# Performance work log

Measured on AMD Instinct MI355X. Metric: run time of the kernel, lower is better.

## Reference

```python
import jax, jax.numpy as jnp
import numpy as np

B, N, DH, DG, HID, K_STEPS, CURV = 256, 2048, 128, 256, 256, 2, 1.0
SC = CURV ** 0.5
SCALE = 1.0 / (DH ** 0.5)
LN_EPS = 1e-5


def _artanh(x):
    return jnp.arctanh(jnp.clip(x, -1.0 + 1e-5, 1.0 - 1e-5))


def logmap0(x, sc=SC):
    n = jnp.maximum(jnp.linalg.norm(x, axis=-1, keepdims=True), 1e-7)
    return x * (_artanh(sc * n) / (sc * n))


def expmap0(v, sc=SC):
    n = jnp.maximum(jnp.linalg.norm(v, axis=-1, keepdims=True), 1e-7)
    return v * (jnp.tanh(sc * n) / (sc * n))


def setup_inputs() -> dict:
    key = jax.random.key(0)
    ks = jax.random.split(key, 16)

    def lin(k, out_d, in_d):
        return (jax.random.normal(k, (out_d, in_d), jnp.float32) * (in_d ** -0.5))

    demo_hyp = expmap0(0.1 * jax.random.normal(ks[0], (B, N, DH), jnp.float32))
    rho_g = jax.random.normal(ks[1], (B, DG), jnp.float32)
    return {
        "demo_hyp": demo_hyp,
        "rho_g": rho_g,
        "seed_g_w": lin(ks[2], DH, DG),
        "seed_g_b": jnp.zeros((DH,), jnp.float32),
        "seed_d_w": lin(ks[3], DH, DH),
        "pool_wq_w": lin(ks[4], DH, DH),
        "pool_wk_w": lin(ks[5], DH, DH),
        "pool_wv_w": lin(ks[6], DH, DH),
        "q_u_w": lin(ks[7], DH, DH),
        "q_g_w": lin(ks[8], DH, DG),
        "q_g_b": jnp.zeros((DH,), jnp.float32),
        "kv_w": lin(ks[9], DH, DH),
        "mlp_w1": lin(ks[10], HID, DH),
        "mlp_b1": jnp.zeros((HID,), jnp.float32),
        "mlp_w2": lin(ks[11], DH, HID),
        "mlp_b2": jnp.zeros((DH,), jnp.float32),
        "ln_g": jnp.ones((DH,), jnp.float32),
        "ln_b": jnp.zeros((DH,), jnp.float32),
    }


def reference(demo_hyp, rho_g, seed_g_w, seed_g_b, seed_d_w,
              pool_wq_w, pool_wk_w, pool_wv_w, q_u_w, q_g_w, q_g_b,
              kv_w, mlp_w1, mlp_b1, mlp_w2, mlp_b2, ln_g, ln_b):
    demo_tan = logmap0(demo_hyp)                       # (B,N,Dh)

    # seed: attention-pool demos with rho_g query
    q_seed = rho_g @ seed_g_w.T + seed_g_b             # (B,Dh)
    qk = q_seed @ pool_wq_w.T                          # (B,Dh)
    Kp = demo_tan @ pool_wk_w.T                        # (B,N,Dh)
    a = jax.nn.softmax(jnp.einsum('bd,bnd->bn', qk, Kp) * SCALE, axis=-1)
    Vp = demo_tan @ pool_wv_w.T
    pooled = jnp.einsum('bn,bnd->bd', a, Vp)           # (B,Dh)
    u = expmap0(q_seed + pooled @ seed_d_w.T)

    for _ in range(K_STEPS):
        u_tan = logmap0(u)
        mu = jnp.mean(u_tan, axis=-1, keepdims=True)
        var = jnp.var(u_tan, axis=-1, keepdims=True)
        u_tan = (u_tan - mu) * jax.lax.rsqrt(var + LN_EPS) * ln_g + ln_b
        q = u_tan @ q_u_w.T + rho_g @ q_g_w.T + q_g_b
        Kmat = demo_tan @ kv_w.T                       # keys == values
        att = jax.nn.softmax(jnp.einsum('bd,bnd->bn', q, Kmat) * SCALE, axis=-1)
        delta = jnp.einsum('bn,bnd->bd', att, Kmat)
        upd = jax.nn.gelu(delta @ mlp_w1.T + mlp_b1, approximate=False) @ mlp_w2.T + mlp_b2
        u = expmap0(u_tan + upd)
    return u
```

## Files before the change

### kernel.cpp

```cpp
#include <hip/hip_runtime.h>
#include <cstddef>
#include <cstdint>

#define B 256
#define N 2048
#define DH 128
#define DG 256
#define HID 256
#define WAVES 8
#define TPB (WAVES * 64)
#define RPI (WAVES * 8)
#define KIT (N / RPI)
#define SCALE 0.08838834764831845f
#define LN_EPS 1e-5f
#define TAN_NORM_MAX 6.2f


__device__ __forceinline__ float artanh_clip(float a) {
  a = fminf(a, 1.0f - 1e-5f);
  return 0.5f * __logf((1.0f + a) / (1.0f - a));
}

__device__ __forceinline__ float logmap_scale(float n2) {
  float nc = fmaxf(sqrtf(n2), 1e-7f);
  return artanh_clip(nc) / nc;
}

__device__ __forceinline__ float row16_sum(float x) {
  x += __int_as_float(__builtin_amdgcn_update_dpp(0, __float_as_int(x), 0x128, 0xF, 0xF, true));
  x += __int_as_float(__builtin_amdgcn_update_dpp(0, __float_as_int(x), 0x124, 0xF, 0xF, true));
  x += __int_as_float(__builtin_amdgcn_update_dpp(0, __float_as_int(x), 0x122, 0xF, 0xF, true));
  x += __int_as_float(__builtin_amdgcn_update_dpp(0, __float_as_int(x), 0x121, 0xF, 0xF, true));
  return x;
}

__device__ __forceinline__ float wave_allsum(float v) {
#pragma unroll
  for (int m = 1; m < 64; m <<= 1) v += __shfl_xor(v, m);
  return v;
}

__device__ __forceinline__ float dot128(const float* __restrict__ wrow,
                                        const float* __restrict__ x) {
  const float4* a = (const float4*)wrow;
  const float4* v = (const float4*)x;
  float s = 0.f;
#pragma unroll
  for (int j = 0; j < 32; ++j) {
    float4 u = a[j], b = v[j];
    s += u.x * b.x + u.y * b.y + u.z * b.z + u.w * b.w;
  }
  return s;
}

__device__ __forceinline__ float dot256(const float* __restrict__ wrow,
                                        const float* __restrict__ x) {
  const float4* a = (const float4*)wrow;
  const float4* v = (const float4*)x;
  float s = 0.f;
#pragma unroll
  for (int j = 0; j < 64; ++j) {
    float4 u = a[j], b = v[j];
    s += u.x * b.x + u.y * b.y + u.z * b.z + u.w * b.w;
  }
  return s;
}


__global__ __launch_bounds__(TPB, 2) void fused_refiner(
    const float* __restrict__ demo, const float* __restrict__ rho,
    const float* __restrict__ seed_g_w, const float* __restrict__ seed_g_b,
    const float* __restrict__ seed_d_w, const float* __restrict__ pool_wq_w,
    const float* __restrict__ pool_wk_w, const float* __restrict__ pool_wv_w,
    const float* __restrict__ q_u_w, const float* __restrict__ q_g_w,
    const float* __restrict__ q_g_b, const float* __restrict__ kv_w,
    const float* __restrict__ mlp_w1, const float* __restrict__ mlp_b1,
    const float* __restrict__ mlp_w2, const float* __restrict__ mlp_b2,
    const float* __restrict__ ln_g, const float* __restrict__ ln_b,
    float* __restrict__ out) {
  const int b = blockIdx.x;
  const int tid = threadIdx.x;
  const int w = tid >> 6;
  const int lane = tid & 63;
  const int g = lane >> 4;
  const int il = lane & 15;

  __shared__ __align__(16) float s_rho[DG];
  __shared__ __align__(16) float s_x[DH];
  __shared__ __align__(16) float s_y[DH];
  __shared__ __align__(16) float s_h[HID];
  __shared__ __align__(16) float s_ut[DH];
  __shared__ __align__(16) float s_qseed[DH];
  __shared__ __align__(16) float s_qvec[DH];
  __shared__ __align__(16) float s_fold[WAVES][DH];
  __shared__ float s_l[WAVES];
  __shared__ float s_red[WAVES];
  __shared__ float s_Mb;

  auto bsumAll = [&](float v) -> float {
    v = wave_allsum(v);
    if (lane == 0) s_red[w] = v;
    __syncthreads();
    float r = s_red[0] + s_red[1] + s_red[2] + s_red[3] +
              s_red[4] + s_red[5] + s_red[6] + s_red[7];
    __syncthreads();
    return r;
  };

  auto ln_query = [&](float v) {
    float n2 = bsumAll(tid < DH ? v * v : 0.f);
    float u = 0.f, ut = 0.f;
    if (tid < DH) {
      float nc = fmaxf(sqrtf(n2), 1e-7f);
      u = v * (tanhf(nc) / nc);
    }
    float nu2 = bsumAll(tid < DH ? u * u : 0.f);
    if (tid < DH) {
      float nuc = fmaxf(sqrtf(nu2), 1e-7f);
      ut = u * (artanh_clip(nuc) / nuc);
    }
    float mu = bsumAll(tid < DH ? ut : 0.f) * (1.0f / DH);
    float d = ut - mu;
    float var = bsumAll(tid < DH ? d * d : 0.f) * (1.0f / DH);
    if (tid < DH) {
      float y = d * rsqrtf(var + LN_EPS) * ln_g[tid] + ln_b[tid];
      s_ut[tid] = y;
      s_x[tid] = y;
    }
    __syncthreads();
    if (tid < DH) {
      s_y[tid] = q_g_b[tid] + dot128(q_u_w + (size_t)tid * DH, s_x) +
                 dot256(q_g_w + (size_t)tid * DG, s_rho);
    }
    __syncthreads();
    float qp = 0.f;
    if (tid < DH) {
#pragma unroll 8
      for (int i = 0; i < DH; ++i) qp += kv_w[i * DH + tid] * s_y[i];
      s_qvec[tid] = qp;
    }
    float qn2 = bsumAll(tid < DH ? qp * qp : 0.f);
    if (tid == 0) s_Mb = SCALE * TAN_NORM_MAX * sqrtf(qn2);
    __syncthreads();
  };

  if (tid < DG) s_rho[tid] = rho[(size_t)b * DG + tid];
  __syncthreads();
  if (tid < DH) {
    float qs = seed_g_b[tid] + dot256(seed_g_w + (size_t)tid * DG, s_rho);
    s_qseed[tid] = qs;
    s_x[tid] = qs;
  }
  __syncthreads();
  if (tid < DH) s_y[tid] = dot128(pool_wq_w + (size_t)tid * DH, s_x);
  __syncthreads();
  float qp0 = 0.f;
  if (tid < DH) {
#pragma unroll 8
    for (int i = 0; i < DH; ++i) qp0 += pool_wk_w[i * DH + tid] * s_y[i];
    s_qvec[tid] = qp0;
  }
  float qn2 = bsumAll(tid < DH ? qp0 * qp0 : 0.f);
  if (tid == 0) s_Mb = SCALE * TAN_NORM_MAX * sqrtf(qn2);
  __syncthreads();

  const float* demo_b = demo + (size_t)b * N * DH;

  for (int pass = 0; pass < 3; ++pass) {
    const float4 qv0 = *(const float4*)&s_qvec[il * 4];
    const float4 qv1 = *(const float4*)&s_qvec[64 + il * 4];
    const float Mb = s_Mb;
    const float* p = demo_b + (size_t)(w * 8 + g) * DH + il * 4;

    float lsum = 0.f;
    float4 accL = make_float4(0.f, 0.f, 0.f, 0.f);
    float4 accH = make_float4(0.f, 0.f, 0.f, 0.f);

    float4 A1[4], A2[4], B1[4], B2[4];
#pragma unroll
    for (int j = 0; j < 3; ++j) {
      const float* pj = p + (size_t)j * RPI * DH;
      A1[j] = *(const float4*)(pj);
      A2[j] = *(const float4*)(pj + 64);
      B1[j] = *(const float4*)(pj + 4 * DH);
      B2[j] = *(const float4*)(pj + 4 * DH + 64);
    }

    for (int kk = 0; kk < KIT; kk += 4) {
#pragma unroll
      for (int j = 0; j < 4; ++j) {
        const int k = kk + j;
        const int jn = (j + 3) & 3;
        if (k + 3 < KIT) {
          const float* pn = p + (size_t)(k + 3) * RPI * DH;
          A1[jn] = *(const float4*)(pn);
          A2[jn] = *(const float4*)(pn + 64);
          B1[jn] = *(const float4*)(pn + 4 * DH);
          B2[jn] = *(const float4*)(pn + 4 * DH + 64);
        }
        float4 ca1 = A1[j], ca2 = A2[j], cb1 = B1[j], cb2 = B2[j];
        {
          float dd = qv0.x * ca1.x + qv0.y * ca1.y + qv0.z * ca1.z + qv0.w * ca1.w +
                     qv1.x * ca2.x + qv1.y * ca2.y + qv1.z * ca2.z + qv1.w * ca2.w;
          float n2 = ca1.x * ca1.x + ca1.y * ca1.y + ca1.z * ca1.z + ca1.w * ca1.w +
                     ca2.x * ca2.x + ca2.y * ca2.y + ca2.z * ca2.z + ca2.w * ca2.w;
          dd = row16_sum(dd);
          n2 = row16_sum(n2);
          float tsv = logmap_scale(n2);
          float pw = __expf(dd * tsv * SCALE - Mb);
          lsum += pw;
          float c = pw * tsv;
          accL.x += c * ca1.x; accL.y += c * ca1.y; accL.z += c * ca1.z; accL.w += c * ca1.w;
          accH.x += c * ca2.x; accH.y += c * ca2.y; accH.z += c * ca2.z; accH.w += c * ca2.w;
        }
        {
          float dd = qv0.x * cb1.x + qv0.y * cb1.y + qv0.z * cb1.z + qv0.w * cb1.w +
                     qv1.x * cb2.x + qv1.y * cb2.y + qv1.z * cb2.z + qv1.w * cb2.w;
          float n2 = cb1.x * cb1.x + cb1.y * cb1.y + cb1.z * cb1.z + cb1.w * cb1.w +
                     cb2.x * cb2.x + cb2.y * cb2.y + cb2.z * cb2.z + cb2.w * cb2.w;
          dd = row16_sum(dd);
          n2 = row16_sum(n2);
          float tsv = logmap_scale(n2);
          float pw = __expf(dd * tsv * SCALE - Mb);
          lsum += pw;
          float c = pw * tsv;
          accL.x += c * cb1.x; accL.y += c * cb1.y; accL.z += c * cb1.z; accL.w += c * cb1.w;
          accH.x += c * cb2.x; accH.y += c * cb2.y; accH.z += c * cb2.z; accH.w += c * cb2.w;
        }
      }
    }

    accL.x += __shfl_xor(accL.x, 16); accL.x += __shfl_xor(accL.x, 32);
    accL.y += __shfl_xor(accL.y, 16); accL.y += __shfl_xor(accL.y, 32);
    accL.z += __shfl_xor(accL.z, 16); accL.z += __shfl_xor(accL.z, 32);
    accL.w += __shfl_xor(accL.w, 16); accL.w += __shfl_xor(accL.w, 32);
    accH.x += __shfl_xor(accH.x, 16); accH.x += __shfl_xor(accH.x, 32);
    accH.y += __shfl_xor(accH.y, 16); accH.y += __shfl_xor(accH.y, 32);
    accH.z += __shfl_xor(accH.z, 16); accH.z += __shfl_xor(accH.z, 32);
    accH.w += __shfl_xor(accH.w, 16); accH.w += __shfl_xor(accH.w, 32);
    lsum += __shfl_xor(lsum, 16); lsum += __shfl_xor(lsum, 32);
    if (g == 0) {
      *(float4*)&s_fold[w][il * 4] = accL;
      *(float4*)&s_fold[w][64 + il * 4] = accH;
      if (il == 0) s_l[w] = lsum;
    }
    __syncthreads();

    if (tid < DH) {
      float a = 0.f;
#pragma unroll
      for (int j = 0; j < WAVES; ++j) a += s_fold[j][tid];
      float L = s_l[0] + s_l[1] + s_l[2] + s_l[3] +
                s_l[4] + s_l[5] + s_l[6] + s_l[7];
      s_x[tid] = a / L;
    }
    __syncthreads();

    if (pass == 0) {
      if (tid < DH) s_y[tid] = dot128(pool_wv_w + (size_t)tid * DH, s_x);
      __syncthreads();
      float v = 0.f;
      if (tid < DH) v = s_qseed[tid] + dot128(seed_d_w + (size_t)tid * DH, s_y);
      ln_query(v);
    } else {
      if (tid < DH) s_y[tid] = dot128(kv_w + (size_t)tid * DH, s_x);
      __syncthreads();
      if (tid < HID) {
        float h = mlp_b1[tid] + dot128(mlp_w1 + (size_t)tid * DH, s_y);
        s_h[tid] = 0.5f * h * (1.0f + erff(h * 0.70710678118654752f));
      }
      __syncthreads();
      float v = 0.f;
      if (tid < DH)
        v = s_ut[tid] + mlp_b2[tid] + dot256(mlp_w2 + (size_t)tid * HID, s_h);
      if (pass == 2) {
        float n2 = bsumAll(tid < DH ? v * v : 0.f);
        if (tid < DH) {
          float nc = fmaxf(sqrtf(n2), 1e-7f);
          out[(size_t)b * DH + tid] = v * (tanhf(nc) / nc);
        }
      } else {
        ln_query(v);
      }
    }
  }
}


extern "C" void kernel_launch(void* const* d_in, const int* in_sizes, int n_in,
                              void* d_out, int out_size, void* d_ws, size_t ws_size,
                              hipStream_t stream) {
  const float* demo      = (const float*)d_in[0];
  const float* rho       = (const float*)d_in[1];
  const float* seed_g_w  = (const float*)d_in[2];
  const float* seed_g_b  = (const float*)d_in[3];
  const float* seed_d_w  = (const float*)d_in[4];
  const float* pool_wq_w = (const float*)d_in[5];
  const float* pool_wk_w = (const float*)d_in[6];
  const float* pool_wv_w = (const float*)d_in[7];
  const float* q_u_w     = (const float*)d_in[8];
  const float* q_g_w     = (const float*)d_in[9];
  const float* q_g_b     = (const float*)d_in[10];
  const float* kv_w      = (const float*)d_in[11];
  const float* mlp_w1    = (const float*)d_in[12];
  const float* mlp_b1    = (const float*)d_in[13];
  const float* mlp_w2    = (const float*)d_in[14];
  const float* mlp_b2    = (const float*)d_in[15];
  const float* ln_g      = (const float*)d_in[16];
  const float* ln_b      = (const float*)d_in[17];
  float* out = (float*)d_out;
  (void)d_ws; (void)ws_size; (void)in_sizes; (void)n_in; (void)out_size;

  fused_refiner<<<B, TPB, 0, stream>>>(demo, rho, seed_g_w, seed_g_b, seed_d_w,
                                       pool_wq_w, pool_wk_w, pool_wv_w, q_u_w,
                                       q_g_w, q_g_b, kv_w, mlp_w1, mlp_b1,
                                       mlp_w2, mlp_b2, ln_g, ln_b, out);
}
```

Before: 532.2 us.

## Cache logmapped demo rows in fp16 workspace for later attention passes

The first pass computes the logmap-scaled demo rows and writes them as fp16 to the workspace. The next two passes stream this half-size cache instead of re-reading fp32 demo and recomputing norms and logmap scales. This cuts global read traffic and per-row ALU work in those passes, at the cost of an extra 128 MB write and fp16 rounding of the keys and values. Launch bounds are also relaxed to one block per CU.

```diff
diff --git a/kernel.cpp b/kernel.cpp
--- a/kernel.cpp
+++ b/kernel.cpp
@@ -1,4 +1,5 @@
 #include <hip/hip_runtime.h>
+#include <hip/hip_fp16.h>
 #include <cstddef>
 #include <cstdint>
 
@@ -67,7 +68,7 @@
 }
 
 
-__global__ __launch_bounds__(TPB, 2) void fused_refiner(
+__global__ __launch_bounds__(TPB, 1) void fused_refiner(
     const float* __restrict__ demo, const float* __restrict__ rho,
     const float* __restrict__ seed_g_w, const float* __restrict__ seed_g_b,
     const float* __restrict__ seed_d_w, const float* __restrict__ pool_wq_w,
@@ -77,7 +78,7 @@
     const float* __restrict__ mlp_w1, const float* __restrict__ mlp_b1,
     const float* __restrict__ mlp_w2, const float* __restrict__ mlp_b2,
     const float* __restrict__ ln_g, const float* __restrict__ ln_b,
-    float* __restrict__ out) {
+    __half* __restrict__ ycache, float* __restrict__ out) {
   const int b = blockIdx.x;
   const int tid = threadIdx.x;
   const int w = tid >> 6;
@@ -165,67 +166,139 @@
   __syncthreads();
 
   const float* demo_b = demo + (size_t)b * N * DH;
+  __half* yc_b = ycache + (size_t)b * N * DH;
 
   for (int pass = 0; pass < 3; ++pass) {
     const float4 qv0 = *(const float4*)&s_qvec[il * 4];
     const float4 qv1 = *(const float4*)&s_qvec[64 + il * 4];
     const float Mb = s_Mb;
-    const float* p = demo_b + (size_t)(w * 8 + g) * DH + il * 4;
 
     float lsum = 0.f;
     float4 accL = make_float4(0.f, 0.f, 0.f, 0.f);
     float4 accH = make_float4(0.f, 0.f, 0.f, 0.f);
 
-    float4 A1[4], A2[4], B1[4], B2[4];
-#pragma unroll
-    for (int j = 0; j < 3; ++j) {
-      const float* pj = p + (size_t)j * RPI * DH;
-      A1[j] = *(const float4*)(pj);
-      A2[j] = *(const float4*)(pj + 64);
-      B1[j] = *(const float4*)(pj + 4 * DH);
-      B2[j] = *(const float4*)(pj + 4 * DH + 64);
-    }
-
-    for (int kk = 0; kk < KIT; kk += 4) {
-#pragma unroll
-      for (int j = 0; j < 4; ++j) {
-        const int k = kk + j;
-        const int jn = (j + 3) & 3;
-        if (k + 3 < KIT) {
-          const float* pn = p + (size_t)(k + 3) * RPI * DH;
-          A1[jn] = *(const float4*)(pn);
-          A2[jn] = *(const float4*)(pn + 64);
-          B1[jn] = *(const float4*)(pn + 4 * DH);
-          B2[jn] = *(const float4*)(pn + 4 * DH + 64);
+    if (pass == 0) {
+      const float* p = demo_b + (size_t)(w * 8 + g) * DH + il * 4;
+      __half* yw = yc_b + (size_t)(w * 8 + g) * DH + (size_t)il * 8;
+
+      float4 A1[4], A2[4], B1[4], B2[4];
+#pragma unroll
+      for (int j = 0; j < 3; ++j) {
+        const float* pj = p + (size_t)j * RPI * DH;
+        A1[j] = *(const float4*)(pj);
+        A2[j] = *(const float4*)(pj + 64);
+        B1[j] = *(const float4*)(pj + 4 * DH);
+        B2[j] = *(const float4*)(pj + 4 * DH + 64);
+      }
+
+      for (int kk = 0; kk < KIT; kk += 4) {
+#pragma unroll
+        for (int j = 0; j < 4; ++j) {
+          const int k = kk + j;
+          const int jn = (j + 3) & 3;
+          if (k + 3 < KIT) {
+            const float* pn = p + (size_t)(k + 3) * RPI * DH;
+            A1[jn] = *(const float4*)(pn);
+            A2[jn] = *(const float4*)(pn + 64);
+            B1[jn] = *(const float4*)(pn + 4 * DH);
+            B2[jn] = *(const float4*)(pn + 4 * DH + 64);
+          }
+          float4 ca1 = A1[j], ca2 = A2[j], cb1 = B1[j], cb2 = B2[j];
+          {
+            float dd = qv0.x * ca1.x + qv0.y * ca1.y + qv0.z * ca1.z + qv0.w * ca1.w +
+                       qv1.x * ca2.x + qv1.y * ca2.y + qv1.z * ca2.z + qv1.w * ca2.w;
+            float n2 = ca1.x * ca1.x + ca1.y * ca1.y + ca1.z * ca1.z + ca1.w * ca1.w +
+                       ca2.x * ca2.x + ca2.y * ca2.y + ca2.z * ca2.z + ca2.w * ca2.w;
+            dd = row16_sum(dd);
+            n2 = row16_sum(n2);
+            float tsv = logmap_scale(n2);
+            float4 y1 = make_float4(tsv * ca1.x, tsv * ca1.y, tsv * ca1.z, tsv * ca1.w);
+            float4 y2 = make_float4(tsv * ca2.x, tsv * ca2.y, tsv * ca2.z, tsv * ca2.w);
+            __half2 h01 = __float22half2_rn(make_float2(y1.x, y1.y));
+            __half2 h23 = __float22half2_rn(make_float2(y1.z, y1.w));
+            __half2 h45 = __float22half2_rn(make_float2(y2.x, y2.y));
+            __half2 h67 = __float22half2_rn(make_float2(y2.z, y2.w));
+            uint4 pk;
+            pk.x = *(const unsigned*)&h01; pk.y = *(const unsigned*)&h23;
+            pk.z = *(const unsigned*)&h45; pk.w = *(const unsigned*)&h67;
+            *(uint4*)(yw + (size_t)k * RPI * DH) = pk;
+            float pw = __expf(dd * tsv * SCALE - Mb);
+            lsum += pw;
+            accL.x += pw * y1.x; accL.y += pw * y1.y; accL.z += pw * y1.z; accL.w += pw * y1.w;
+            accH.x += pw * y2.x; accH.y += pw * y2.y; accH.z += pw * y2.z; accH.w += pw * y2.w;
+          }
+          {
+            float dd = qv0.x * cb1.x + qv0.y * cb1.y + qv0.z * cb1.z + qv0.w * cb1.w +
+                       qv1.x * cb2.x + qv1.y * cb2.y + qv1.z * cb2.z + qv1.w * cb2.w;
+            float n2 = cb1.x * cb1.x + cb1.y * cb1.y + cb1.z * cb1.z + cb1.w * cb1.w +
+                       cb2.x * cb2.x + cb2.y * cb2.y + cb2.z * cb2.z + cb2.w * cb2.w;
+            dd = row16_sum(dd);
+            n2 = row16_sum(n2);
+            float tsv = logmap_scale(n2);
+            float4 y1 = make_float4(tsv * cb1.x, tsv * cb1.y, tsv * cb1.z, tsv * cb1.w);
+            float4 y2 = make_float4(tsv * cb2.x, tsv * cb2.y, tsv * cb2.z, tsv * cb2.w);
+            __half2 h01 = __float22half2_rn(make_float2(y1.x, y1.y));
+            __half2 h23 = __float22half2_rn(make_float2(y1.z, y1.w));
+            __half2 h45 = __float22half2_rn(make_float2(y2.x, y2.y));
+            __half2 h67 = __float22half2_rn(make_float2(y2.z, y2.w));
+            uint4 pk;
+            pk.x = *(const unsigned*)&h01; pk.y = *(const unsigned*)&h23;
+            pk.z = *(const unsigned*)&h45; pk.w = *(const unsigned*)&h67;
+            *(uint4*)(yw + (size_t)k * RPI * DH + 4 * DH) = pk;
+            float pw = __expf(dd * tsv * SCALE - Mb);
+            lsum += pw;
+            accL.x += pw * y1.x; accL.y += pw * y1.y; accL.z += pw * y1.z; accL.w += pw * y1.w;
+            accH.x += pw * y2.x; accH.y += pw * y2.y; accH.z += pw * y2.z; accH.w += pw * y2.w;
+          }
         }
-        float4 ca1 = A1[j], ca2 = A2[j], cb1 = B1[j], cb2 = B2[j];
-        {
-          float dd = qv0.x * ca1.x + qv0.y * ca1.y + qv0.z * ca1.z + qv0.w * ca1.w +
-                     qv1.x * ca2.x + qv1.y * ca2.y + qv1.z * ca2.z + qv1.w * ca2.w;
-          float n2 = ca1.x * ca1.x + ca1.y * ca1.y + ca1.z * ca1.z + ca1.w * ca1.w +
-                     ca2.x * ca2.x + ca2.y * ca2.y + ca2.z * ca2.z + ca2.w * ca2.w;
-          dd = row16_sum(dd);
-          n2 = row16_sum(n2);
-          float tsv = logmap_scale(n2);
-          float pw = __expf(dd * tsv * SCALE - Mb);
-          lsum += pw;
-          float c = pw * tsv;
-          accL.x += c * ca1.x; accL.y += c * ca1.y; accL.z += c * ca1.z; accL.w += c * ca1.w;
-          accH.x += c * ca2.x; accH.y += c * ca2.y; accH.z += c * ca2.z; accH.w += c * ca2.w;
-        }
-        {
-          float dd = qv0.x * cb1.x + qv0.y * cb1.y + qv0.z * cb1.z + qv0.w * cb1.w +
-                     qv1.x * cb2.x + qv1.y * cb2.y + qv1.z * cb2.z + qv1.w * cb2.w;
-          float n2 = cb1.x * cb1.x + cb1.y * cb1.y + cb1.z * cb1.z + cb1.w * cb1.w +
-                     cb2.x * cb2.x + cb2.y * cb2.y + cb2.z * cb2.z + cb2.w * cb2.w;
-          dd = row16_sum(dd);
-          n2 = row16_sum(n2);
-          float tsv = logmap_scale(n2);
-          float pw = __expf(dd * tsv * SCALE - Mb);
-          lsum += pw;
-          float c = pw * tsv;
-          accL.x += c * cb1.x; accL.y += c * cb1.y; accL.z += c * cb1.z; accL.w += c * cb1.w;
-          accH.x += c * cb2.x; accH.y += c * cb2.y; accH.z += c * cb2.z; accH.w += c * cb2.w;
+      }
+    } else {
+      const __half* yr = yc_b + (size_t)(w * 8 + g) * DH + (size_t)il * 8;
+
+      uint4 YA[4], YB[4];
+#pragma unroll
+      for (int j = 0; j < 3; ++j) {
+        YA[j] = *(const uint4*)(yr + (size_t)j * RPI * DH);
+        YB[j] = *(const uint4*)(yr + (size_t)j * RPI * DH + 4 * DH);
+      }
+
+      for (int kk = 0; kk < KIT; kk += 4) {
+#pragma unroll
+        for (int j = 0; j < 4; ++j) {
+          const int k = kk + j;
+          const int jn = (j + 3) & 3;
+          if (k + 3 < KIT) {
+            YA[jn] = *(const uint4*)(yr + (size_t)(k + 3) * RPI * DH);
+            YB[jn] = *(const uint4*)(yr + (size_t)(k + 3) * RPI * DH + 4 * DH);
+          }
+          {
+            uint4 pk = YA[j];
+            float2 f0 = __half22float2(*(const __half2*)&pk.x);
+            float2 f1 = __half22float2(*(const __half2*)&pk.y);
+            float2 f2 = __half22float2(*(const __half2*)&pk.z);
+            float2 f3 = __half22float2(*(const __half2*)&pk.w);
+            float dd = qv0.x * f0.x + qv0.y * f0.y + qv0.z * f1.x + qv0.w * f1.y +
+                       qv1.x * f2.x + qv1.y * f2.y + qv1.z * f3.x + qv1.w * f3.y;
+            dd = row16_sum(dd);
+            float pw = __expf(dd * SCALE - Mb);
+            lsum += pw;
+            accL.x += pw * f0.x; accL.y += pw * f0.y; accL.z += pw * f1.x; accL.w += pw * f1.y;
+            accH.x += pw * f2.x; accH.y += pw * f2.y; accH.z += pw * f3.x; accH.w += pw * f3.y;
+          }
+          {
+            uint4 pk = YB[j];
+            float2 f0 = __half22float2(*(const __half2*)&pk.x);
+            float2 f1 = __half22float2(*(const __half2*)&pk.y);
+            float2 f2 = __half22float2(*(const __half2*)&pk.z);
+            float2 f3 = __half22float2(*(const __half2*)&pk.w);
+            float dd = qv0.x * f0.x + qv0.y * f0.y + qv0.z * f1.x + qv0.w * f1.y +
+                       qv1.x * f2.x + qv1.y * f2.y + qv1.z * f3.x + qv1.w * f3.y;
+            dd = row16_sum(dd);
+            float pw = __expf(dd * SCALE - Mb);
+            lsum += pw;
+            accL.x += pw * f0.x; accL.y += pw * f0.y; accL.z += pw * f1.x; accL.w += pw * f1.y;
+            accH.x += pw * f2.x; accH.y += pw * f2.y; accH.z += pw * f3.x; accH.w += pw * f3.y;
+          }
         }
       }
     }
@@ -309,10 +382,11 @@
   const float* ln_g      = (const float*)d_in[16];
   const float* ln_b      = (const float*)d_in[17];
   float* out = (float*)d_out;
-  (void)d_ws; (void)ws_size; (void)in_sizes; (void)n_in; (void)out_size;
+  __half* ycache = (__half*)d_ws;
+  (void)ws_size; (void)in_sizes; (void)n_in; (void)out_size;
 
   fused_refiner<<<B, TPB, 0, stream>>>(demo, rho, seed_g_w, seed_g_b, seed_d_w,
                                        pool_wq_w, pool_wk_w, pool_wv_w, q_u_w,
                                        q_g_w, q_g_b, kv_w, mlp_w1, mlp_b1,
-                                       mlp_w2, mlp_b2, ln_g, ln_b, out);
-}
+                                       mlp_w2, mlp_b2, ln_g, ln_b, ycache, out);
+}
```

Result: faster. 519.3 us (-2.4%).
